# Kernel optimization log

Measured on AMD Instinct MI355X. Metric: run time of the kernel, lower is better.

The kernel has to match this reference:

```python
import jax, jax.numpy as jnp
from jax import lax
import numpy as np

C_IN, C_OUT, K, STRIDE, PAD = 64, 64, 3, 1, 1
EPS = 1e-5


def setup_inputs() -> dict:
    key = jax.random.key(0)
    ks = jax.random.split(key, 6)
    B, H, W = 4, 128, 128
    x = jax.random.normal(ks[0], (B, C_IN, H, W), jnp.float32)
    # small offset weights -> realistic sub-pixel offsets
    offset_w = jax.random.normal(ks[1], (2 * K * K, C_IN, K, K), jnp.float32) * 0.01
    offset_b = jax.random.normal(ks[2], (2 * K * K,), jnp.float32) * 0.01
    dcn_w = jax.random.normal(ks[3], (C_OUT, C_IN, K, K), jnp.float32) / np.sqrt(C_IN * K * K)
    gamma = jax.random.uniform(ks[4], (C_OUT,), jnp.float32, 0.5, 1.5)
    beta = jax.random.normal(ks[5], (C_OUT,), jnp.float32) * 0.1
    return dict(x=x, offset_w=offset_w, offset_b=offset_b, dcn_w=dcn_w, gamma=gamma, beta=beta)


def _bilinear_sample(xb, py, px):
    # xb: (C,H,W); py,px: (K2,Ho,Wo) absolute sample coords (may be out of bounds)
    H, W = xb.shape[1], xb.shape[2]
    y0 = jnp.floor(py); x0 = jnp.floor(px)
    wy = py - y0  # frac weights
    wx = px - x0

    def gather(yi, xi):
        yc = jnp.clip(yi, 0, H - 1).astype(jnp.int32)
        xc = jnp.clip(xi, 0, W - 1).astype(jnp.int32)
        v = xb[:, yc, xc]  # (C,K2,Ho,Wo)
        valid = ((yi >= 0) & (yi <= H - 1) & (xi >= 0) & (xi <= W - 1)).astype(xb.dtype)
        return v * valid[None]

    return (gather(y0, x0) * ((1 - wy) * (1 - wx))[None]
            + gather(y0, x0 + 1) * ((1 - wy) * wx)[None]
            + gather(y0 + 1, x0) * (wy * (1 - wx))[None]
            + gather(y0 + 1, x0 + 1) * (wy * wx)[None])  # (C,K2,Ho,Wo)


def reference(x, offset_w, offset_b, dcn_w, gamma, beta):
    B, C, H, W = x.shape
    K2 = K * K
    # offset conv (standard conv, NCHW)
    offset = lax.conv_general_dilated(
        x, offset_w, (STRIDE, STRIDE), [(PAD, PAD), (PAD, PAD)],
        dimension_numbers=("NCHW", "OIHW", "NCHW")) + offset_b[None, :, None, None]
    Ho, Wo = offset.shape[2], offset.shape[3]
    off = offset.reshape(B, K2, 2, Ho, Wo)  # interleaved (dy, dx) per tap
    dy, dx = off[:, :, 0], off[:, :, 1]
    # base sampling grid: out_pos*stride - pad + kernel tap index
    hs = (jnp.arange(Ho) * STRIDE - PAD).astype(x.dtype)
    ws = (jnp.arange(Wo) * STRIDE - PAD).astype(x.dtype)
    ki, kj = jnp.meshgrid(jnp.arange(K), jnp.arange(K), indexing="ij")
    ki = ki.reshape(K2).astype(x.dtype)
    kj = kj.reshape(K2).astype(x.dtype)
    py = dy + hs[None, None, :, None] + ki[None, :, None, None]  # (B,K2,Ho,Wo)
    px = dx + ws[None, None, None, :] + kj[None, :, None, None]

    sampled = jax.vmap(_bilinear_sample)(x, py, px)  # (B,C,K2,Ho,Wo)
    out = jnp.einsum("bckhw,ock->bohw", sampled, dcn_w.reshape(dcn_w.shape[0], C, K2))

    # BatchNorm (training-mode batch stats) + ReLU
    mean = out.mean((0, 2, 3))
    var = out.var((0, 2, 3))
    out = (out - mean[None, :, None, None]) * lax.rsqrt(var + EPS)[None, :, None, None]
    out = out * gamma[None, :, None, None] + beta[None, :, None, None]
    return jnp.maximum(out, 0.0)
```

## Files before the change

kernel.cpp:

```cpp
#include <hip/hip_runtime.h>

#define HW   16384
#define NPX  65536

typedef unsigned short u16;
typedef unsigned int   u32;
typedef short bf16x8 __attribute__((ext_vector_type(8)));
typedef float f32x4  __attribute__((ext_vector_type(4)));

__device__ __forceinline__ u16 f2b(float f) {
    u32 u = __float_as_uint(f);
    return (u16)((u + 0x7FFFu + ((u >> 16) & 1u)) >> 16);
}
__device__ __forceinline__ float blo(u32 u) { return __uint_as_float(u << 16); }
__device__ __forceinline__ float bhi(u32 u) { return __uint_as_float(u & 0xffff0000u); }

__device__ __forceinline__ u32 comb(u32 a00, u32 a01, u32 a10, u32 a11,
                                    float w00, float w01, float w10, float w11) {
    float lo = fmaf(w11, blo(a11), fmaf(w10, blo(a10), fmaf(w01, blo(a01), w00 * blo(a00))));
    float hi = fmaf(w11, bhi(a11), fmaf(w10, bhi(a10), fmaf(w01, bhi(a01), w00 * bhi(a00))));
    return __builtin_amdgcn_perm(__float_as_uint(hi) + 0x8000u,
                                 __float_as_uint(lo) + 0x8000u, 0x07060302u);
}
__device__ __forceinline__ bf16x8 comb4(int4 v00, int4 v01, int4 v10, int4 v11,
                                        float w00, float w01, float w10, float w11) {
    int4 r;
    r.x = comb(v00.x, v01.x, v10.x, v11.x, w00, w01, w10, w11);
    r.y = comb(v00.y, v01.y, v10.y, v11.y, w00, w01, w10, w11);
    r.z = comb(v00.z, v01.z, v10.z, v11.z, w00, w01, w10, w11);
    r.w = comb(v00.w, v01.w, v10.w, v11.w, w00, w01, w10, w11);
    return __builtin_bit_cast(bf16x8, r);
}

#define MFMA __builtin_amdgcn_mfma_f32_16x16x32_bf16

__global__ __launch_bounds__(256)
void k_pre(const float* __restrict__ x, const float* __restrict__ dw,
           const float* __restrict__ ow, u16* __restrict__ xh,
           u16* __restrict__ wtd, u16* __restrict__ wto,
           float* __restrict__ sums) {
    int tid = threadIdx.x;
    int bid = blockIdx.x;
    if (bid >= 512) {
        if (bid == 539) {
            for (int i = tid; i < 1024; i += 256) sums[i] = 0.f;
            return;
        }
        int gid = (bid - 512) * 256 + tid;
        if (gid >= 108 * 64) return;
        int fid = gid >> 6, lane = gid & 63;
        int mi = lane & 15, quad = lane >> 4;
        u32 w[4];
        if (fid < 72) {
            int tap = fid >> 3, rem = fid & 7;
            int ks = rem >> 2, nt = rem & 3;
            int n = nt * 16 + mi;
            int cb = ks * 32 + quad * 8;
#pragma unroll
            for (int i = 0; i < 4; ++i) {
                u32 lo = f2b(dw[(n * 64 + cb + 2 * i) * 9 + tap]);
                u32 hi = f2b(dw[(n * 64 + cb + 2 * i + 1) * 9 + tap]);
                w[i] = lo | (hi << 16);
            }
            *((int4*)wtd + (fid << 6) + lane) = make_int4(w[0], w[1], w[2], w[3]);
        } else {
            int f2 = fid - 72;
            int tap = f2 >> 2, rem = f2 & 3;
            int ks = rem >> 1, nt = rem & 1;
            int n = nt * 16 + mi;
            int cb = ks * 32 + quad * 8;
#pragma unroll
            for (int i = 0; i < 4; ++i) {
                u32 lo = (n < 18) ? f2b(ow[(n * 64 + cb + 2 * i) * 9 + tap]) : 0u;
                u32 hi = (n < 18) ? f2b(ow[(n * 64 + cb + 2 * i + 1) * 9 + tap]) : 0u;
                w[i] = lo | (hi << 16);
            }
            *((int4*)wto + (f2 << 6) + lane) = make_int4(w[0], w[1], w[2], w[3]);
        }
        return;
    }
    __shared__ u16 tile[64][138];
    int p0  = bid * 128;
    int b   = p0 >> 14;
    int hw0 = p0 & (HW - 1);
    int pxq = (tid & 31) * 4;
    int rr  = tid >> 5;
    const float* src = x + (size_t)b * 64 * HW + hw0 + pxq;
#pragma unroll
    for (int i = 0; i < 8; ++i) {
        int c = i * 8 + rr;
        float4 v = *(const float4*)(src + (size_t)c * HW);
        ushort4 h;
        h.x = f2b(v.x); h.y = f2b(v.y); h.z = f2b(v.z); h.w = f2b(v.w);
        *(ushort4*)&tile[c][pxq] = h;
    }
    __syncthreads();
    int sub = tid & 3;
#pragma unroll
    for (int j = 0; j < 2; ++j) {
        int px = j * 64 + (tid >> 2);
        u32 w[8];
#pragma unroll
        for (int t = 0; t < 8; ++t) {
            int c = sub * 16 + 2 * t;
            w[t] = (u32)tile[c][px] | ((u32)tile[c + 1][px] << 16);
        }
        u16* dst = xh + (size_t)(p0 + px) * 64 + sub * 16;
        *(int4*)dst       = make_int4(w[0], w[1], w[2], w[3]);
        *(int4*)(dst + 8) = make_int4(w[4], w[5], w[6], w[7]);
    }
}

__global__ __launch_bounds__(256, 5)
void k_main(const u16* __restrict__ xh, const u16* __restrict__ wto,
            const u16* __restrict__ wtd, const float* __restrict__ ob,
            float* __restrict__ out, float* __restrict__ sums) {
    __shared__ float offs[2][18][34];
    __shared__ float so[64][33];

    int tid = threadIdx.x;
    int vb  = (blockIdx.x & 7) * 256 + (blockIdx.x >> 3);
    int p0  = vb * 32;
    int b   = p0 >> 14;
    int hw0 = p0 & (HW - 1);
    int y   = hw0 >> 7;
    int x0  = hw0 & 127;
    int wave = tid >> 6, lane = tid & 63;
    int mi = lane & 15, quad = lane >> 4;
    int ks = wave >> 1;
    int m0 = (wave & 1) << 4;
    int xcol = x0 + m0 + mi;
    int koff = ks * 32 + quad * 8;
    const u16* xb = xh + (size_t)b * HW * 64;
    const bf16x8* WO = (const bf16x8*)wto;
    const bf16x8* WD = (const bf16x8*)wtd;

    int4 av[9];
#pragma unroll
    for (int tap = 0; tap < 9; ++tap) {
        int yy = y + tap / 3 - 1;
        int xx = xcol + tap % 3 - 1;
        int yc = min(max(yy, 0), 127), xc = min(max(xx, 0), 127);
        int4 a = *(const int4*)(xb + ((yc << 7) + xc) * 64 + koff);
        if (!(((unsigned)yy < 128u) && ((unsigned)xx < 128u)))
            a = make_int4(0, 0, 0, 0);
        av[tap] = a;
    }
    f32x4 oa0 = {0.f, 0.f, 0.f, 0.f}, oa1 = {0.f, 0.f, 0.f, 0.f};
#pragma unroll
    for (int tap = 0; tap < 9; ++tap) {
        bf16x8 af = __builtin_bit_cast(bf16x8, av[tap]);
        oa0 = MFMA(af, WO[((tap * 4 + ks * 2 + 0) << 6) + lane], oa0, 0, 0, 0);
        oa1 = MFMA(af, WO[((tap * 4 + ks * 2 + 1) << 6) + lane], oa1, 0, 0, 0);
    }
    {
        float bias0 = (ks == 0) ? ob[mi] : 0.f;
#pragma unroll
        for (int r = 0; r < 4; ++r)
            offs[ks][mi][m0 + quad * 4 + r] = oa0[r] + bias0;
        if (mi < 2) {
            float bias1 = (ks == 0) ? ob[16 + mi] : 0.f;
#pragma unroll
            for (int r = 0; r < 4; ++r)
                offs[ks][16 + mi][m0 + quad * 4 + r] = oa1[r] + bias1;
        }
    }
    __syncthreads();

    int pxl = m0 + mi;
    float offv[18];
#pragma unroll
    for (int m = 0; m < 18; ++m)
        offv[m] = offs[0][m][pxl] + offs[1][m][pxl];

    float fy = (float)y, fx = (float)xcol;
    f32x4 acc0 = {0.f,0.f,0.f,0.f}, acc1 = {0.f,0.f,0.f,0.f};
    f32x4 acc2 = {0.f,0.f,0.f,0.f}, acc3 = {0.f,0.f,0.f,0.f};

#pragma unroll
    for (int bt = 0; bt < 5; ++bt) {
        const int ntap = (bt == 4) ? 1 : 2;
        int4  vv[8];
        float wts[2][4];
#pragma unroll
        for (int j = 0; j < 2; ++j) {
            if (j < ntap) {
                int tap = bt * 2 + j;
                float py  = offv[2 * tap]     + fy + (float)(tap / 3 - 1);
                float pf  = offv[2 * tap + 1] + fx + (float)(tap % 3 - 1);
                float y0f = floorf(py), x0f = floorf(pf);
                float wy  = py - y0f,   wx  = pf - x0f;
                int   iy0 = (int)y0f,   ix0 = (int)x0f;
                float vy0 = (y0f >=  0.f && y0f <= 127.f) ? 1.f : 0.f;
                float vy1 = (y0f >= -1.f && y0f <= 126.f) ? 1.f : 0.f;
                float vx0 = (x0f >=  0.f && x0f <= 127.f) ? 1.f : 0.f;
                float vx1 = (x0f >= -1.f && x0f <= 126.f) ? 1.f : 0.f;
                int cy0 = min(max(iy0, 0), 127), cy1 = min(max(iy0 + 1, 0), 127);
                int cx0 = min(max(ix0, 0), 127), cx1 = min(max(ix0 + 1, 0), 127);
                wts[j][0] = (1.f - wy) * (1.f - wx) * vy0 * vx0;
                wts[j][1] = (1.f - wy) * wx * vy0 * vx1;
                wts[j][2] = wy * (1.f - wx) * vy1 * vx0;
                wts[j][3] = wy * wx * vy1 * vx1;
                vv[j * 4 + 0] = *(const int4*)(xb + ((cy0 << 7) + cx0) * 64 + koff);
                vv[j * 4 + 1] = *(const int4*)(xb + ((cy0 << 7) + cx1) * 64 + koff);
                vv[j * 4 + 2] = *(const int4*)(xb + ((cy1 << 7) + cx0) * 64 + koff);
                vv[j * 4 + 3] = *(const int4*)(xb + ((cy1 << 7) + cx1) * 64 + koff);
            }
        }
        __builtin_amdgcn_sched_barrier(0);
#pragma unroll
        for (int j = 0; j < 2; ++j) {
            if (j < ntap) {
                int tap = bt * 2 + j;
                bf16x8 a = comb4(vv[j * 4 + 0], vv[j * 4 + 1],
                                 vv[j * 4 + 2], vv[j * 4 + 3],
                                 wts[j][0], wts[j][1], wts[j][2], wts[j][3]);
                acc0 = MFMA(a, WD[((tap * 8 + ks * 4 + 0) << 6) + lane], acc0, 0, 0, 0);
                acc1 = MFMA(a, WD[((tap * 8 + ks * 4 + 1) << 6) + lane], acc1, 0, 0, 0);
                acc2 = MFMA(a, WD[((tap * 8 + ks * 4 + 2) << 6) + lane], acc2, 0, 0, 0);
                acc3 = MFMA(a, WD[((tap * 8 + ks * 4 + 3) << 6) + lane], acc3, 0, 0, 0);
            }
        }
    }

    if (ks == 1) {
#pragma unroll
        for (int r = 0; r < 4; ++r) {
            so[ 0 + mi][m0 + quad * 4 + r] = acc0[r];
            so[16 + mi][m0 + quad * 4 + r] = acc1[r];
            so[32 + mi][m0 + quad * 4 + r] = acc2[r];
            so[48 + mi][m0 + quad * 4 + r] = acc3[r];
        }
    }
    __syncthreads();
    if (ks == 0) {
#pragma unroll
        for (int r = 0; r < 4; ++r) {
            so[ 0 + mi][m0 + quad * 4 + r] += acc0[r];
            so[16 + mi][m0 + quad * 4 + r] += acc1[r];
            so[32 + mi][m0 + quad * 4 + r] += acc2[r];
            so[48 + mi][m0 + quad * 4 + r] += acc3[r];
        }
    }
    __syncthreads();

    int n  = tid >> 2;
    int c4 = tid & 3;
    int pl = c4 * 8;
    float s = 0.f, q = 0.f;
    float vals[8];
#pragma unroll
    for (int i = 0; i < 8; ++i) {
        float v = so[n][pl + i];
        vals[i] = v;
        s += v;
        q = fmaf(v, v, q);
    }
    float* dst = out + (size_t)(b * 64 + n) * HW + (y << 7) + x0 + pl;
    *(float4*)dst       = make_float4(vals[0], vals[1], vals[2], vals[3]);
    *(float4*)(dst + 4) = make_float4(vals[4], vals[5], vals[6], vals[7]);

    s += __shfl_xor(s, 1); s += __shfl_xor(s, 2);
    q += __shfl_xor(q, 1); q += __shfl_xor(q, 2);
    if (c4 == 0) {
        float* sb = sums + (blockIdx.x & 7) * 128;
        atomicAdd(&sb[n], s);
        atomicAdd(&sb[64 + n], q);
    }
}

__global__ __launch_bounds__(256)
void k_bn(float* __restrict__ out, const float* __restrict__ sums,
          const float* __restrict__ gamma, const float* __restrict__ beta) {
    int i4 = blockIdx.x * 256 + threadIdx.x;
    int e  = i4 << 2;
    int o  = (e >> 14) & 63;
    float sm = 0.f, sq = 0.f;
#pragma unroll
    for (int s8 = 0; s8 < 8; ++s8) {
        sm += sums[s8 * 128 + o];
        sq += sums[s8 * 128 + 64 + o];
    }
    const float n = 65536.f;
    float mean = sm / n;
    float var  = fmaxf(sq / n - mean * mean, 0.f);
    float sc   = rsqrtf(var + 1e-5f) * gamma[o];
    float sh   = beta[o] - mean * sc;
    float4 v = *(const float4*)&out[e];
    v.x = fmaxf(fmaf(v.x, sc, sh), 0.f);
    v.y = fmaxf(fmaf(v.y, sc, sh), 0.f);
    v.z = fmaxf(fmaf(v.z, sc, sh), 0.f);
    v.w = fmaxf(fmaf(v.w, sc, sh), 0.f);
    *(float4*)&out[e] = v;
}

extern "C" void kernel_launch(void* const* d_in, const int* in_sizes, int n_in,
                              void* d_out, int out_size, void* d_ws, size_t ws_size,
                              hipStream_t stream) {
    const float* x     = (const float*)d_in[0];
    const float* ow    = (const float*)d_in[1];
    const float* ob    = (const float*)d_in[2];
    const float* dw    = (const float*)d_in[3];
    const float* gamma = (const float*)d_in[4];
    const float* beta  = (const float*)d_in[5];
    float* out = (float*)d_out;
    char*  wsb = (char*)d_ws;
    u16*   xh   = (u16*)wsb;
    u16*   wtd  = (u16*)(wsb + 8388608);
    u16*   wto  = (u16*)(wsb + 8462336);
    float* sums = (float*)(wsb + 8499200);

    k_pre<<<540, 256, 0, stream>>>(x, dw, ow, xh, wtd, wto, sums);
    k_main<<<2048, 256, 0, stream>>>(xh, wto, wtd, ob, out, sums);
    k_bn<<<4096, 256, 0, stream>>>(out, sums, gamma, beta);
}
```

Before: 147.2 us.

## Drop explicit tap batching, raise occupancy bound, use nontemporal weight loads

Removes the two-tap batching with sched_barrier and the preloaded av[9] array, turning both the offset conv and the deformable sampling into simple per-tap loops. Raises the launch-bounds minimum blocks per SM from 5 to 6 to reduce register usage and gain occupancy. Loads MFMA weight fragments with nontemporal hints. This gives up explicit latency hiding within a wave and relies on extra waves and the compiler scheduler instead. Nontemporal hints on heavily reused weights may also cost cache hits.

```diff
diff --git a/kernel.cpp b/kernel.cpp
--- a/kernel.cpp
+++ b/kernel.cpp
@@ -22,17 +22,9 @@
     return __builtin_amdgcn_perm(__float_as_uint(hi) + 0x8000u,
                                  __float_as_uint(lo) + 0x8000u, 0x07060302u);
 }
-__device__ __forceinline__ bf16x8 comb4(int4 v00, int4 v01, int4 v10, int4 v11,
-                                        float w00, float w01, float w10, float w11) {
-    int4 r;
-    r.x = comb(v00.x, v01.x, v10.x, v11.x, w00, w01, w10, w11);
-    r.y = comb(v00.y, v01.y, v10.y, v11.y, w00, w01, w10, w11);
-    r.z = comb(v00.z, v01.z, v10.z, v11.z, w00, w01, w10, w11);
-    r.w = comb(v00.w, v01.w, v10.w, v11.w, w00, w01, w10, w11);
-    return __builtin_bit_cast(bf16x8, r);
-}
 
 #define MFMA __builtin_amdgcn_mfma_f32_16x16x32_bf16
+#define NTL(p) __builtin_nontemporal_load(p)
 
 __global__ __launch_bounds__(256)
 void k_pre(const float* __restrict__ x, const float* __restrict__ dw,
@@ -111,7 +103,7 @@
     }
 }
 
-__global__ __launch_bounds__(256, 5)
+__global__ __launch_bounds__(256, 6)
 void k_main(const u16* __restrict__ xh, const u16* __restrict__ wto,
             const u16* __restrict__ wtd, const float* __restrict__ ob,
             float* __restrict__ out, float* __restrict__ sums) {
@@ -135,23 +127,18 @@
     const bf16x8* WO = (const bf16x8*)wto;
     const bf16x8* WD = (const bf16x8*)wtd;
 
-    int4 av[9];
+    f32x4 oa0 = {0.f, 0.f, 0.f, 0.f}, oa1 = {0.f, 0.f, 0.f, 0.f};
 #pragma unroll
     for (int tap = 0; tap < 9; ++tap) {
         int yy = y + tap / 3 - 1;
         int xx = xcol + tap % 3 - 1;
         int yc = min(max(yy, 0), 127), xc = min(max(xx, 0), 127);
+        bool valid = ((unsigned)yy < 128u) && ((unsigned)xx < 128u);
         int4 a = *(const int4*)(xb + ((yc << 7) + xc) * 64 + koff);
-        if (!(((unsigned)yy < 128u) && ((unsigned)xx < 128u)))
-            a = make_int4(0, 0, 0, 0);
-        av[tap] = a;
-    }
-    f32x4 oa0 = {0.f, 0.f, 0.f, 0.f}, oa1 = {0.f, 0.f, 0.f, 0.f};
-#pragma unroll
-    for (int tap = 0; tap < 9; ++tap) {
-        bf16x8 af = __builtin_bit_cast(bf16x8, av[tap]);
-        oa0 = MFMA(af, WO[((tap * 4 + ks * 2 + 0) << 6) + lane], oa0, 0, 0, 0);
-        oa1 = MFMA(af, WO[((tap * 4 + ks * 2 + 1) << 6) + lane], oa1, 0, 0, 0);
+        if (!valid) a = make_int4(0, 0, 0, 0);
+        bf16x8 af = __builtin_bit_cast(bf16x8, a);
+        oa0 = MFMA(af, NTL(&WO[((tap * 4 + ks * 2 + 0) << 6) + lane]), oa0, 0, 0, 0);
+        oa1 = MFMA(af, NTL(&WO[((tap * 4 + ks * 2 + 1) << 6) + lane]), oa1, 0, 0, 0);
     }
     {
         float bias0 = (ks == 0) ? ob[mi] : 0.f;
@@ -178,49 +165,36 @@
     f32x4 acc2 = {0.f,0.f,0.f,0.f}, acc3 = {0.f,0.f,0.f,0.f};
 
 #pragma unroll
-    for (int bt = 0; bt < 5; ++bt) {
-        const int ntap = (bt == 4) ? 1 : 2;
-        int4  vv[8];
-        float wts[2][4];
-#pragma unroll
-        for (int j = 0; j < 2; ++j) {
-            if (j < ntap) {
-                int tap = bt * 2 + j;
-                float py  = offv[2 * tap]     + fy + (float)(tap / 3 - 1);
-                float pf  = offv[2 * tap + 1] + fx + (float)(tap % 3 - 1);
-                float y0f = floorf(py), x0f = floorf(pf);
-                float wy  = py - y0f,   wx  = pf - x0f;
-                int   iy0 = (int)y0f,   ix0 = (int)x0f;
-                float vy0 = (y0f >=  0.f && y0f <= 127.f) ? 1.f : 0.f;
-                float vy1 = (y0f >= -1.f && y0f <= 126.f) ? 1.f : 0.f;
-                float vx0 = (x0f >=  0.f && x0f <= 127.f) ? 1.f : 0.f;
-                float vx1 = (x0f >= -1.f && x0f <= 126.f) ? 1.f : 0.f;
-                int cy0 = min(max(iy0, 0), 127), cy1 = min(max(iy0 + 1, 0), 127);
-                int cx0 = min(max(ix0, 0), 127), cx1 = min(max(ix0 + 1, 0), 127);
-                wts[j][0] = (1.f - wy) * (1.f - wx) * vy0 * vx0;
-                wts[j][1] = (1.f - wy) * wx * vy0 * vx1;
-                wts[j][2] = wy * (1.f - wx) * vy1 * vx0;
-                wts[j][3] = wy * wx * vy1 * vx1;
-                vv[j * 4 + 0] = *(const int4*)(xb + ((cy0 << 7) + cx0) * 64 + koff);
-                vv[j * 4 + 1] = *(const int4*)(xb + ((cy0 << 7) + cx1) * 64 + koff);
-                vv[j * 4 + 2] = *(const int4*)(xb + ((cy1 << 7) + cx0) * 64 + koff);
-                vv[j * 4 + 3] = *(const int4*)(xb + ((cy1 << 7) + cx1) * 64 + koff);
-            }
-        }
-        __builtin_amdgcn_sched_barrier(0);
-#pragma unroll
-        for (int j = 0; j < 2; ++j) {
-            if (j < ntap) {
-                int tap = bt * 2 + j;
-                bf16x8 a = comb4(vv[j * 4 + 0], vv[j * 4 + 1],
-                                 vv[j * 4 + 2], vv[j * 4 + 3],
-                                 wts[j][0], wts[j][1], wts[j][2], wts[j][3]);
-                acc0 = MFMA(a, WD[((tap * 8 + ks * 4 + 0) << 6) + lane], acc0, 0, 0, 0);
-                acc1 = MFMA(a, WD[((tap * 8 + ks * 4 + 1) << 6) + lane], acc1, 0, 0, 0);
-                acc2 = MFMA(a, WD[((tap * 8 + ks * 4 + 2) << 6) + lane], acc2, 0, 0, 0);
-                acc3 = MFMA(a, WD[((tap * 8 + ks * 4 + 3) << 6) + lane], acc3, 0, 0, 0);
-            }
-        }
+    for (int tap = 0; tap < 9; ++tap) {
+        float py  = offv[2 * tap]     + fy + (float)(tap / 3 - 1);
+        float pf  = offv[2 * tap + 1] + fx + (float)(tap % 3 - 1);
+        float y0f = floorf(py), x0f = floorf(pf);
+        float wy  = py - y0f,   wx  = pf - x0f;
+        int   iy0 = (int)y0f,   ix0 = (int)x0f;
+        float vy0 = (y0f >=  0.f && y0f <= 127.f) ? 1.f : 0.f;
+        float vy1 = (y0f >= -1.f && y0f <= 126.f) ? 1.f : 0.f;
+        float vx0 = (x0f >=  0.f && x0f <= 127.f) ? 1.f : 0.f;
+        float vx1 = (x0f >= -1.f && x0f <= 126.f) ? 1.f : 0.f;
+        int cy0 = min(max(iy0, 0), 127), cy1 = min(max(iy0 + 1, 0), 127);
+        int cx0 = min(max(ix0, 0), 127), cx1 = min(max(ix0 + 1, 0), 127);
+        float w00 = (1.f - wy) * (1.f - wx) * vy0 * vx0;
+        float w01 = (1.f - wy) * wx * vy0 * vx1;
+        float w10 = wy * (1.f - wx) * vy1 * vx0;
+        float w11 = wy * wx * vy1 * vx1;
+        int4 v00 = *(const int4*)(xb + ((cy0 << 7) + cx0) * 64 + koff);
+        int4 v01 = *(const int4*)(xb + ((cy0 << 7) + cx1) * 64 + koff);
+        int4 v10 = *(const int4*)(xb + ((cy1 << 7) + cx0) * 64 + koff);
+        int4 v11 = *(const int4*)(xb + ((cy1 << 7) + cx1) * 64 + koff);
+        int4 r;
+        r.x = comb(v00.x, v01.x, v10.x, v11.x, w00, w01, w10, w11);
+        r.y = comb(v00.y, v01.y, v10.y, v11.y, w00, w01, w10, w11);
+        r.z = comb(v00.z, v01.z, v10.z, v11.z, w00, w01, w10, w11);
+        r.w = comb(v00.w, v01.w, v10.w, v11.w, w00, w01, w10, w11);
+        bf16x8 a = __builtin_bit_cast(bf16x8, r);
+        acc0 = MFMA(a, NTL(&WD[((tap * 8 + ks * 4 + 0) << 6) + lane]), acc0, 0, 0, 0);
+        acc1 = MFMA(a, NTL(&WD[((tap * 8 + ks * 4 + 1) << 6) + lane]), acc1, 0, 0, 0);
+        acc2 = MFMA(a, NTL(&WD[((tap * 8 + ks * 4 + 2) << 6) + lane]), acc2, 0, 0, 0);
+        acc3 = MFMA(a, NTL(&WD[((tap * 8 + ks * 4 + 3) << 6) + lane]), acc3, 0, 0, 0);
     }
 
     if (ks == 1) {
```

Result: no change. 144.9 us (-1.6%).
